# Optimization experiments

Hardware: AMD Instinct MI355X
Metric: run time of the kernel (lower is better)

Reference implementation:

```python
import jax, jax.numpy as jnp
import numpy as np

IOU_THR = 0.5
TOP_K = 10
D_MODEL = 256
BS, NQ = 8, 1000


def _layer_norm(x, g, b, eps=1e-5):
    m = x.mean(-1, keepdims=True)
    v = ((x - m) ** 2).mean(-1, keepdims=True)
    return (x - m) * jax.lax.rsqrt(v + eps) * g + b


def _box_iou(boxes):
    # boxes: [nq, 4] xyxy; pairwise IoU [nq, nq]
    area = (boxes[:, 2] - boxes[:, 0]) * (boxes[:, 3] - boxes[:, 1])
    lt = jnp.maximum(boxes[:, None, :2], boxes[None, :, :2])
    rb = jnp.minimum(boxes[:, None, 2:], boxes[None, :, 2:])
    wh = jnp.clip(rb - lt, 0.0)
    inter = wh[..., 0] * wh[..., 1]
    union = area[:, None] + area[None, :] - inter
    return inter / union


def setup_inputs() -> dict:
    key = jax.random.key(0)
    ks = jax.random.split(key, 16)
    d = D_MODEL
    s = 1.0 / np.sqrt(d)
    tgt = jax.random.normal(ks[0], (BS, NQ, d), dtype=jnp.float32)
    seed_mask = (jax.random.uniform(ks[1], (BS, NQ, 1)) < 0.2).astype(jnp.float32)
    # cxcywh boxes in (0,1) with positive wh
    cxy = jax.random.uniform(ks[2], (BS, NQ, 2), minval=0.1, maxval=0.9)
    wh = jax.random.uniform(ks[3], (BS, NQ, 2), minval=0.05, maxval=0.3)
    pred_boxes = jnp.concatenate([cxy, wh], axis=-1).astype(jnp.float32)
    def lin(k):
        kw, kb = jax.random.split(k)
        return (jax.random.uniform(kw, (d, d), minval=-s, maxval=s, dtype=jnp.float32),
                jax.random.uniform(kb, (d,), minval=-s, maxval=s, dtype=jnp.float32))
    W1, b1 = lin(ks[4]); W2, b2 = lin(ks[5]); W3, b3 = lin(ks[6])
    W4, b4 = lin(ks[7]); W5, b5 = lin(ks[8])
    g2 = jnp.ones((d,), jnp.float32); be2 = jnp.zeros((d,), jnp.float32)
    return {"tgt": tgt, "seed_mask": seed_mask, "pred_boxes": pred_boxes,
            "W1": W1, "b1": b1, "W2": W2, "b2": b2, "g2": g2, "be2": be2,
            "W3": W3, "b3": b3, "W4": W4, "b4": b4, "W5": W5, "b5": b5}


def reference(tgt, seed_mask, pred_boxes, W1, b1, W2, b2, g2, be2, W3, b3, W4, b4, W5, b5):
    bs, nq, d = tgt.shape
    # cxcywh -> xyxy
    cxy, wh = pred_boxes[..., :2], pred_boxes[..., 2:]
    box_xyxy = jnp.concatenate([cxy - 0.5 * wh, cxy + 0.5 * wh], axis=-1)
    ious = jax.vmap(_box_iou)(box_xyxy)                       # [bs,nq,nq]
    attn_mask = ious >= IOU_THR
    neg_mask = 1.0 - seed_mask                                # [bs,nq,1]
    # mask out non-seed columns and seed rows
    overlaps = ious * jnp.swapaxes(seed_mask, 1, 2) * neg_mask  # [bs,nq,nq]
    idx = jnp.argsort(-overlaps, axis=-1)[..., :TOP_K]        # [bs,nq,k]
    nmk = jnp.take_along_axis(
        jnp.broadcast_to(jnp.swapaxes(seed_mask, 1, 2), (bs, nq, nq)), idx, axis=2)
    ious_g = jnp.take_along_axis(overlaps, idx, axis=2)       # [bs,nq,k]
    mk = nmk * (ious_g >= IOU_THR).astype(tgt.dtype)          # [bs,nq,k]
    # id token MLP + layernorm
    id_token = _layer_norm(jax.nn.relu(tgt @ W1 + b1) @ W2 + b2, g2, be2)
    # neighbor gather: [bs,nq,k,d]
    neighbors_id = jax.vmap(lambda t, i: t[i])(id_token, idx)
    id_feature = id_token[:, :, None, :] - neighbors_id
    features = jax.nn.relu(id_feature @ W3 + b3) @ W4 + b4
    cur_tgt = (features * mk[..., None]).max(axis=2)          # [bs,nq,d]
    cur_tgt = tgt + jax.nn.relu(cur_tgt @ W5 + b5) * neg_mask
    return cur_tgt, attn_mask
```

## Files before the change

### kernel.cpp

```cpp
#include <hip/hip_runtime.h>
#include <hip/hip_bf16.h>

#define BSZ   8
#define NQ    1000
#define DM    256
#define MROWS (BSZ*NQ)
#define TOPK  10

typedef __attribute__((ext_vector_type(8))) short short8;
typedef __attribute__((ext_vector_type(4))) float f32x4;
typedef unsigned short u16;
typedef unsigned int   u32;

static __device__ __forceinline__ float b2f(u16 u) { return __uint_as_float(((u32)u) << 16); }
static __device__ __forceinline__ u16 f2b(float f) {
    __hip_bfloat16 h = __float2bfloat16(f);
    return *(u16*)&h;
}
static __device__ __forceinline__ u32 encf(float f) {
    u32 u = __float_as_uint(f);
    return (u & 0x80000000u) ? ~u : (u | 0x80000000u);
}
static __device__ __forceinline__ float decf(u32 e) {
    u32 u = (e & 0x80000000u) ? (e ^ 0x80000000u) : ~e;
    return __uint_as_float(u);
}

__global__ __launch_bounds__(256) void prep_iou_k(
    const float* __restrict__ boxes, const float* __restrict__ seed,
    const float* __restrict__ W1, const float* __restrict__ W2,
    const float* __restrict__ W3, const float* __restrict__ W4,
    const float* __restrict__ W5, u16* __restrict__ WT,
    float* __restrict__ attn, int* __restrict__ cnt,
    int* __restrict__ inc0, int* __restrict__ idxs)
{
#pragma clang fp contract(off)
    if (blockIdx.x < 80) {
        const int m  = blockIdx.x >> 4;
        const int kb = (blockIdx.x & 15) * 16;
        const float* W = (m==0)?W1:(m==1)?W2:(m==2)?W3:(m==3)?W4:W5;
        u16* D = WT + (size_t)m * DM * DM;
        const int t = threadIdx.x;
        u16 tmp[16];
        #pragma unroll
        for (int kk = 0; kk < 16; ++kk)
            tmp[kk] = f2b(W[(size_t)(kb+kk)*DM + t]);
        #pragma unroll
        for (int kk = 0; kk < 16; ++kk)
            D[(size_t)t*DM + kb + kk] = tmp[kk];
        return;
    }

    __shared__ float sv[NQ];
    __shared__ int   sj[NQ];
    __shared__ int   scount;
    const int t   = threadIdx.x;
    const int row = blockIdx.x - 80;
    const int b   = row / NQ;
    if (t == 0) scount = 0;

    const float* bi = boxes + (size_t)row * 4;
    const float icx = bi[0], icy = bi[1], iw = bi[2], ih = bi[3];
    const float ix0 = icx - 0.5f*iw, iy0 = icy - 0.5f*ih;
    const float ix1 = icx + 0.5f*iw, iy1 = icy + 0.5f*ih;
    const float area_i = (ix1-ix0)*(iy1-iy0);
    const float neg_i  = 1.f - seed[row];
    __syncthreads();

    float* arow = attn + (size_t)row * NQ;
    for (int j = t; j < NQ; j += 256) {
        const float* bj = boxes + (size_t)(b*NQ + j) * 4;
        const float cx = bj[0], cy = bj[1], w = bj[2], h = bj[3];
        const float x0 = cx - 0.5f*w, y0 = cy - 0.5f*h;
        const float x1 = cx + 0.5f*w, y1 = cy + 0.5f*h;
        const float area_j = (x1-x0)*(y1-y0);
        const float ltx = fmaxf(ix0, x0), lty = fmaxf(iy0, y0);
        const float rbx = fminf(ix1, x1), rby = fminf(iy1, y1);
        const float wx = fmaxf(rbx-ltx, 0.f), wy = fmaxf(rby-lty, 0.f);
        const float inter = wx*wy;
        const float uni = (area_i + area_j) - inter;
        const float iou = inter / uni;
        arow[j] = (iou >= 0.5f) ? 1.0f : 0.0f;
        const float ov = (iou * seed[b*NQ + j]) * neg_i;
        if (ov >= 0.5f) {
            const int p = atomicAdd(&scount, 1);
            if (p < NQ) { sv[p] = ov; sj[p] = j; }
        }
    }
    __syncthreads();

    if (t == 0) {
        const int n = scount;
        inc0[row] = (n < TOPK) ? 1 : 0;
        if (n <= TOPK) {
            cnt[row] = n;
            for (int k = 0; k < n; ++k) idxs[row*TOPK + k] = b*NQ + sj[k];
        } else {
            float bv[TOPK]; int bj[TOPK];
            #pragma unroll
            for (int k = 0; k < TOPK; ++k) { bv[k] = -1.f; bj[k] = 0x7fffffff; }
            for (int e = 0; e < n; ++e) {
                const float v = sv[e]; const int j = sj[e];
                int w = 0;
                #pragma unroll
                for (int k = 1; k < TOPK; ++k)
                    if (bv[k] < bv[w] || (bv[k] == bv[w] && bj[k] > bj[w])) w = k;
                if (v > bv[w] || (v == bv[w] && j < bj[w])) { bv[w] = v; bj[w] = j; }
            }
            cnt[row] = TOPK;
            for (int k = 0; k < TOPK; ++k) idxs[row*TOPK + k] = b*NQ + bj[k];
        }
    }
}

template<int EPI>
static __device__ __forceinline__ void block_gemm256(
    const u16 (*__restrict__ A)[264], const u16* __restrict__ WT,
    const float* __restrict__ bias, u16 (*__restrict__ OutL)[264],
    u16* __restrict__ OutG, float* __restrict__ OutF,
    const float* __restrict__ tgt, const float* __restrict__ seed,
    int r0, u16 (*__restrict__ W_lds)[72], int t)
{
    const int lane = t & 63, wave = t >> 6;
    const int m = lane & 15, quad = lane >> 4;
    f32x4 acc[4];
    #pragma unroll
    for (int nt = 0; nt < 4; ++nt)
        #pragma unroll
        for (int i = 0; i < 4; ++i) acc[nt][i] = 0.f;
    for (int kc = 0; kc < 4; ++kc) {
        __syncthreads();
        #pragma unroll
        for (int pass = 0; pass < 8; ++pass) {
            const int n = pass*32 + (t >> 3), ko = (t & 7) * 8;
            *(uint4*)&W_lds[n][ko] = *(const uint4*)&WT[(size_t)n*DM + kc*64 + ko];
        }
        __syncthreads();
        #pragma unroll
        for (int ks = 0; ks < 2; ++ks) {
            const short8 a = *(const short8*)&A[m][kc*64 + ks*32 + quad*8];
            #pragma unroll
            for (int nt = 0; nt < 4; ++nt) {
                const int n = wave*64 + nt*16 + m;
                const short8 b = *(const short8*)&W_lds[n][ks*32 + quad*8];
                acc[nt] = __builtin_amdgcn_mfma_f32_16x16x32_bf16(a, b, acc[nt], 0, 0, 0);
            }
        }
    }
    #pragma unroll
    for (int nt = 0; nt < 4; ++nt) {
        const int n = wave*64 + nt*16 + m;
        const float bb = bias ? bias[n] : 0.f;
        #pragma unroll
        for (int reg = 0; reg < 4; ++reg) {
            const int rl = quad*4 + reg;
            float v = acc[nt][reg] + bb;
            if (EPI == 0) OutL[rl][n] = f2b(fmaxf(v, 0.f));
            if (EPI == 1) OutL[rl][n] = f2b(v);
            if (EPI == 2) OutG[(size_t)(r0+rl)*DM + n] = f2b(v);
            if (EPI == 3) {
                const int R = r0 + rl;
                OutF[(size_t)R*DM + n] = tgt[(size_t)R*DM + n]
                                       + fmaxf(v, 0.f) * (1.f - seed[R]);
            }
        }
    }
}

__global__ __launch_bounds__(256) void mlp_k(
    const float* __restrict__ tgt, const u16* __restrict__ WT,
    const float* __restrict__ b1, const float* __restrict__ b2,
    const float* __restrict__ g2, const float* __restrict__ be2,
    u16* __restrict__ P)
{
    __shared__ __align__(16) u16 bufA[16][264];
    __shared__ __align__(16) u16 bufB[16][264];
    __shared__ __align__(16) u16 W_lds[256][72];
    const int t = threadIdx.x, r0 = blockIdx.x * 16;
    const int lane = t & 63, wave = t >> 6;

    {
        const int r = t >> 4, c0 = (t & 15) * 16;
        const float* src = &tgt[(size_t)(r0 + r)*DM + c0];
        u16 h[16];
        #pragma unroll
        for (int q = 0; q < 4; ++q) {
            const float4 f = *(const float4*)&src[q*4];
            h[q*4+0] = f2b(f.x); h[q*4+1] = f2b(f.y);
            h[q*4+2] = f2b(f.z); h[q*4+3] = f2b(f.w);
        }
        *(uint4*)&bufA[r][c0]     = *(uint4*)&h[0];
        *(uint4*)&bufA[r][c0 + 8] = *(uint4*)&h[8];
    }
    const u16* W1T = WT;
    const u16* W2T = WT + (size_t)1*DM*DM;
    const u16* W3T = WT + (size_t)2*DM*DM;

    block_gemm256<0>(bufA, W1T, b1, bufB, nullptr, nullptr, nullptr, nullptr, r0, W_lds, t);
    block_gemm256<1>(bufB, W2T, b2, bufA, nullptr, nullptr, nullptr, nullptr, r0, W_lds, t);
    __syncthreads();
    for (int rr = 0; rr < 4; ++rr) {
        const int row = wave*4 + rr;
        float x[4];
        #pragma unroll
        for (int i = 0; i < 4; ++i) x[i] = b2f(bufA[row][lane + 64*i]);
        float s = x[0]+x[1]+x[2]+x[3];
        float q = x[0]*x[0]+x[1]*x[1]+x[2]*x[2]+x[3]*x[3];
        #pragma unroll
        for (int off = 32; off; off >>= 1) {
            s += __shfl_down(s, off, 64);
            q += __shfl_down(q, off, 64);
        }
        s = __shfl(s, 0, 64); q = __shfl(q, 0, 64);
        const float mn  = s * (1.f/DM);
        const float vr  = q * (1.f/DM) - mn*mn;
        const float inv = rsqrtf(vr + 1e-5f);
        #pragma unroll
        for (int i = 0; i < 4; ++i) {
            const int c = lane + 64*i;
            bufA[row][c] = f2b((x[i]-mn)*inv*g2[c] + be2[c]);
        }
    }
    block_gemm256<2>(bufA, W3T, nullptr, nullptr, P, nullptr, nullptr, nullptr, r0, W_lds, t);
}

__global__ __launch_bounds__(256) void pairs_final_k(
    const u16* __restrict__ P, const u16* __restrict__ WT,
    const float* __restrict__ b3, const float* __restrict__ b4,
    const float* __restrict__ b5,
    const int* __restrict__ cnt, const int* __restrict__ inc0,
    const int* __restrict__ idxs,
    const float* __restrict__ tgt, const float* __restrict__ seed,
    float* __restrict__ out)
{
    __shared__ __align__(16) u16 U[16][264];
    __shared__ __align__(16) u16 W_lds[256][72];
    __shared__ u32 cmU[16][264];
    __shared__ int pl_rl[176], pl_j[176];
    __shared__ int sInc[16];
    __shared__ int np;
    const int t = threadIdx.x, r0 = blockIdx.x * 16;
    const int lane = t & 63, wave = t >> 6;
    const int m = lane & 15, quad = lane >> 4;
    const u16* W4T = WT + (size_t)3*DM*DM;
    const u16* W5T = WT + (size_t)4*DM*DM;

    if (t == 0) np = 0;
    __syncthreads();
    if (t < 16) {
        const int r = r0 + t;
        int c = cnt[r];
        c = (c < 0) ? 0 : ((c > TOPK) ? TOPK : c);
        sInc[t] = inc0[r];
        const int base = atomicAdd(&np, c);
        for (int k = 0; k < c; ++k) {
            pl_rl[base + k] = t;
            int j = idxs[r*TOPK + k];
            j = (j < 0) ? 0 : ((j >= MROWS) ? MROWS-1 : j);
            pl_j[base + k] = j;
        }
    }
    __syncthreads();
    const int npairs = np;
    #pragma unroll
    for (int rl2 = 0; rl2 < 16; ++rl2)
        cmU[rl2][t] = sInc[rl2] ? 0x80000000u  : encf(-3.402823466e38f);
    const float bb3 = b3[t];

    for (int pc = 0; pc*16 < npairs; ++pc) {
        #pragma unroll
        for (int pp = 0; pp < 16; ++pp) {
            const int pr = pc*16 + pp;
            u16 uv = 0;
            if (pr < npairs) {
                const int i = r0 + pl_rl[pr];
                const int j = pl_j[pr];
                uv = f2b(fmaxf(b2f(P[(size_t)i*DM + t]) - b2f(P[(size_t)j*DM + t]) + bb3, 0.f));
            }
            U[pp][t] = uv;
        }
        f32x4 acc[4];
        #pragma unroll
        for (int nt = 0; nt < 4; ++nt)
            #pragma unroll
            for (int i = 0; i < 4; ++i) acc[nt][i] = 0.f;
        for (int kc = 0; kc < 4; ++kc) {
            __syncthreads();
            #pragma unroll
            for (int pass = 0; pass < 8; ++pass) {
                const int n = pass*32 + (t >> 3), ko = (t & 7) * 8;
                *(uint4*)&W_lds[n][ko] = *(const uint4*)&W4T[(size_t)n*DM + kc*64 + ko];
            }
            __syncthreads();
            #pragma unroll
            for (int ks = 0; ks < 2; ++ks) {
                const short8 a = *(const short8*)&U[m][kc*64 + ks*32 + quad*8];
                #pragma unroll
                for (int nt = 0; nt < 4; ++nt) {
                    const int n = wave*64 + nt*16 + m;
                    const short8 b = *(const short8*)&W_lds[n][ks*32 + quad*8];
                    acc[nt] = __builtin_amdgcn_mfma_f32_16x16x32_bf16(a, b, acc[nt], 0, 0, 0);
                }
            }
        }
        #pragma unroll
        for (int nt = 0; nt < 4; ++nt) {
            const int n = wave*64 + nt*16 + m;
            const float bb4 = b4[n];
            #pragma unroll
            for (int reg = 0; reg < 4; ++reg) {
                const int pr = pc*16 + quad*4 + reg;
                if (pr < npairs) {
                    const int rl2 = pl_rl[pr];
                    atomicMax(&cmU[rl2][n], encf(acc[nt][reg] + bb4));
                }
            }
        }
    }
    __syncthreads();
    #pragma unroll
    for (int rl2 = 0; rl2 < 16; ++rl2)
        U[rl2][t] = f2b(decf(cmU[rl2][t]));
    block_gemm256<3>(U, W5T, b5, nullptr, nullptr, out, tgt, seed, r0, W_lds, t);
}

extern "C" void kernel_launch(void* const* d_in, const int* in_sizes, int n_in,
                              void* d_out, int out_size, void* d_ws, size_t ws_size,
                              hipStream_t stream)
{
    (void)in_sizes; (void)n_in; (void)out_size; (void)ws_size;
    const float* tgt   = (const float*)d_in[0];
    const float* seed  = (const float*)d_in[1];
    const float* boxes = (const float*)d_in[2];
    const float* W1 = (const float*)d_in[3];
    const float* b1 = (const float*)d_in[4];
    const float* W2 = (const float*)d_in[5];
    const float* b2 = (const float*)d_in[6];
    const float* g2 = (const float*)d_in[7];
    const float* be2= (const float*)d_in[8];
    const float* W3 = (const float*)d_in[9];
    const float* b3 = (const float*)d_in[10];
    const float* W4 = (const float*)d_in[11];
    const float* b4 = (const float*)d_in[12];
    const float* W5 = (const float*)d_in[13];
    const float* b5 = (const float*)d_in[14];

    float* out_tgt  = (float*)d_out;
    float* out_attn = out_tgt + (size_t)MROWS * DM;

    u16* WT   = (u16*)d_ws;
    u16* P    = WT + (size_t)5*DM*DM;
    int* cnt  = (int*)(P + (size_t)MROWS*DM);
    int* inc0 = cnt + MROWS;
    int* idxs = inc0 + MROWS;

    prep_iou_k<<<80 + MROWS, 256, 0, stream>>>(boxes, seed, W1, W2, W3, W4, W5,
                                               WT, out_attn, cnt, inc0, idxs);
    mlp_k<<<MROWS/16, 256, 0, stream>>>(tgt, WT, b1, b2, g2, be2, P);
    pairs_final_k<<<MROWS/16, 256, 0, stream>>>(P, WT, b3, b4, b5, cnt, inc0, idxs,
                                                tgt, seed, out_tgt);
}
```

Measured before the change: 141.7 us.

## Run IoU/top-k blocks concurrently with MLP blocks in one fused launch

Moves the weight transpose into its own small kernel and merges the per-row IoU/top-k work with the id-token MLP into one launch whose blocks branch on block index, sharing a union-style shared-memory buffer. The aim is to overlap the latency-bound IoU blocks with the MFMA-heavy MLP tiles instead of running them in series. The trade-off is that shared-memory footprint per block becomes the MLP size for the IoU blocks too, which may reduce occupancy for the 8000 IoU blocks.

```diff
diff --git a/kernel.cpp b/kernel.cpp
--- a/kernel.cpp
+++ b/kernel.cpp
@@ -6,6 +6,7 @@
 #define DM    256
 #define MROWS (BSZ*NQ)
 #define TOPK  10
+#define NTILE (MROWS/16)
 
 typedef __attribute__((ext_vector_type(8))) short short8;
 typedef __attribute__((ext_vector_type(4))) float f32x4;
@@ -26,91 +27,23 @@
     return __uint_as_float(u);
 }
 
-__global__ __launch_bounds__(256) void prep_iou_k(
-    const float* __restrict__ boxes, const float* __restrict__ seed,
+__global__ __launch_bounds__(256) void prep_k(
     const float* __restrict__ W1, const float* __restrict__ W2,
     const float* __restrict__ W3, const float* __restrict__ W4,
-    const float* __restrict__ W5, u16* __restrict__ WT,
-    float* __restrict__ attn, int* __restrict__ cnt,
-    int* __restrict__ inc0, int* __restrict__ idxs)
-{
-#pragma clang fp contract(off)
-    if (blockIdx.x < 80) {
-        const int m  = blockIdx.x >> 4;
-        const int kb = (blockIdx.x & 15) * 16;
-        const float* W = (m==0)?W1:(m==1)?W2:(m==2)?W3:(m==3)?W4:W5;
-        u16* D = WT + (size_t)m * DM * DM;
-        const int t = threadIdx.x;
-        u16 tmp[16];
-        #pragma unroll
-        for (int kk = 0; kk < 16; ++kk)
-            tmp[kk] = f2b(W[(size_t)(kb+kk)*DM + t]);
-        #pragma unroll
-        for (int kk = 0; kk < 16; ++kk)
-            D[(size_t)t*DM + kb + kk] = tmp[kk];
-        return;
-    }
-
-    __shared__ float sv[NQ];
-    __shared__ int   sj[NQ];
-    __shared__ int   scount;
-    const int t   = threadIdx.x;
-    const int row = blockIdx.x - 80;
-    const int b   = row / NQ;
-    if (t == 0) scount = 0;
-
-    const float* bi = boxes + (size_t)row * 4;
-    const float icx = bi[0], icy = bi[1], iw = bi[2], ih = bi[3];
-    const float ix0 = icx - 0.5f*iw, iy0 = icy - 0.5f*ih;
-    const float ix1 = icx + 0.5f*iw, iy1 = icy + 0.5f*ih;
-    const float area_i = (ix1-ix0)*(iy1-iy0);
-    const float neg_i  = 1.f - seed[row];
-    __syncthreads();
-
-    float* arow = attn + (size_t)row * NQ;
-    for (int j = t; j < NQ; j += 256) {
-        const float* bj = boxes + (size_t)(b*NQ + j) * 4;
-        const float cx = bj[0], cy = bj[1], w = bj[2], h = bj[3];
-        const float x0 = cx - 0.5f*w, y0 = cy - 0.5f*h;
-        const float x1 = cx + 0.5f*w, y1 = cy + 0.5f*h;
-        const float area_j = (x1-x0)*(y1-y0);
-        const float ltx = fmaxf(ix0, x0), lty = fmaxf(iy0, y0);
-        const float rbx = fminf(ix1, x1), rby = fminf(iy1, y1);
-        const float wx = fmaxf(rbx-ltx, 0.f), wy = fmaxf(rby-lty, 0.f);
-        const float inter = wx*wy;
-        const float uni = (area_i + area_j) - inter;
-        const float iou = inter / uni;
-        arow[j] = (iou >= 0.5f) ? 1.0f : 0.0f;
-        const float ov = (iou * seed[b*NQ + j]) * neg_i;
-        if (ov >= 0.5f) {
-            const int p = atomicAdd(&scount, 1);
-            if (p < NQ) { sv[p] = ov; sj[p] = j; }
-        }
-    }
-    __syncthreads();
-
-    if (t == 0) {
-        const int n = scount;
-        inc0[row] = (n < TOPK) ? 1 : 0;
-        if (n <= TOPK) {
-            cnt[row] = n;
-            for (int k = 0; k < n; ++k) idxs[row*TOPK + k] = b*NQ + sj[k];
-        } else {
-            float bv[TOPK]; int bj[TOPK];
-            #pragma unroll
-            for (int k = 0; k < TOPK; ++k) { bv[k] = -1.f; bj[k] = 0x7fffffff; }
-            for (int e = 0; e < n; ++e) {
-                const float v = sv[e]; const int j = sj[e];
-                int w = 0;
-                #pragma unroll
-                for (int k = 1; k < TOPK; ++k)
-                    if (bv[k] < bv[w] || (bv[k] == bv[w] && bj[k] > bj[w])) w = k;
-                if (v > bv[w] || (v == bv[w] && j < bj[w])) { bv[w] = v; bj[w] = j; }
-            }
-            cnt[row] = TOPK;
-            for (int k = 0; k < TOPK; ++k) idxs[row*TOPK + k] = b*NQ + bj[k];
-        }
-    }
+    const float* __restrict__ W5, u16* __restrict__ WT)
+{
+    const int m  = blockIdx.x >> 4;
+    const int kb = (blockIdx.x & 15) * 16;
+    const float* W = (m==0)?W1:(m==1)?W2:(m==2)?W3:(m==3)?W4:W5;
+    u16* D = WT + (size_t)m * DM * DM;
+    const int t = threadIdx.x;
+    u16 tmp[16];
+    #pragma unroll
+    for (int kk = 0; kk < 16; ++kk)
+        tmp[kk] = f2b(W[(size_t)(kb+kk)*DM + t]);
+    #pragma unroll
+    for (int kk = 0; kk < 16; ++kk)
+        D[(size_t)t*DM + kb + kk] = tmp[kk];
 }
 
 template<int EPI>
@@ -167,61 +100,136 @@
     }
 }
 
-__global__ __launch_bounds__(256) void mlp_k(
-    const float* __restrict__ tgt, const u16* __restrict__ WT,
+struct MlpSmem { u16 bufA[16][264]; u16 bufB[16][264]; u16 W_lds[256][72]; };
+struct IouSmem { float sv[NQ]; int sj[NQ]; int scount; };
+
+__global__ __launch_bounds__(256) void fused_iou_mlp_k(
+    const float* __restrict__ boxes, const float* __restrict__ seed,
+    const u16* __restrict__ WT,
     const float* __restrict__ b1, const float* __restrict__ b2,
     const float* __restrict__ g2, const float* __restrict__ be2,
-    u16* __restrict__ P)
-{
-    __shared__ __align__(16) u16 bufA[16][264];
-    __shared__ __align__(16) u16 bufB[16][264];
-    __shared__ __align__(16) u16 W_lds[256][72];
-    const int t = threadIdx.x, r0 = blockIdx.x * 16;
-    const int lane = t & 63, wave = t >> 6;
+    const float* __restrict__ tgt,
+    u16* __restrict__ P, float* __restrict__ attn,
+    int* __restrict__ cnt, int* __restrict__ inc0, int* __restrict__ idxs)
+{
+    __shared__ __align__(16) unsigned char smraw[sizeof(MlpSmem)];
+    const int t = threadIdx.x;
+    const int bid = blockIdx.x;
+
+    if (bid < NTILE) {
+        MlpSmem& sm = *reinterpret_cast<MlpSmem*>(smraw);
+        const int r0 = bid * 16;
+        const int lane = t & 63, wave = t >> 6;
+        const u16* W1T = WT;
+        const u16* W2T = WT + (size_t)1*DM*DM;
+        const u16* W3T = WT + (size_t)2*DM*DM;
+
+        {
+            const int r = t >> 4, c0 = (t & 15) * 16;
+            const float* src = &tgt[(size_t)(r0 + r)*DM + c0];
+            __align__(16) u16 h[16];
+            #pragma unroll
+            for (int q = 0; q < 4; ++q) {
+                const float4 f = *(const float4*)&src[q*4];
+                h[q*4+0] = f2b(f.x); h[q*4+1] = f2b(f.y);
+                h[q*4+2] = f2b(f.z); h[q*4+3] = f2b(f.w);
+            }
+            *(uint4*)&sm.bufA[r][c0]     = *(uint4*)&h[0];
+            *(uint4*)&sm.bufA[r][c0 + 8] = *(uint4*)&h[8];
+        }
+
+        block_gemm256<0>(sm.bufA, W1T, b1, sm.bufB,
+                         nullptr, nullptr, nullptr, nullptr, r0, sm.W_lds, t);
+        block_gemm256<1>(sm.bufB, W2T, b2, sm.bufA,
+                         nullptr, nullptr, nullptr, nullptr, r0, sm.W_lds, t);
+        __syncthreads();
+        for (int rr = 0; rr < 4; ++rr) {
+            const int row = wave*4 + rr;
+            float x[4];
+            #pragma unroll
+            for (int i = 0; i < 4; ++i) x[i] = b2f(sm.bufA[row][lane + 64*i]);
+            float s = x[0]+x[1]+x[2]+x[3];
+            float q = x[0]*x[0]+x[1]*x[1]+x[2]*x[2]+x[3]*x[3];
+            #pragma unroll
+            for (int off = 32; off; off >>= 1) {
+                s += __shfl_down(s, off, 64);
+                q += __shfl_down(q, off, 64);
+            }
+            s = __shfl(s, 0, 64); q = __shfl(q, 0, 64);
+            const float mn  = s * (1.f/DM);
+            const float vr  = q * (1.f/DM) - mn*mn;
+            const float inv = rsqrtf(vr + 1e-5f);
+            #pragma unroll
+            for (int i = 0; i < 4; ++i) {
+                const int c = lane + 64*i;
+                sm.bufA[row][c] = f2b((x[i]-mn)*inv*g2[c] + be2[c]);
+            }
+        }
+        block_gemm256<2>(sm.bufA, W3T, nullptr, nullptr,
+                         P, nullptr, nullptr, nullptr, r0, sm.W_lds, t);
+        return;
+    }
 
     {
-        const int r = t >> 4, c0 = (t & 15) * 16;
-        const float* src = &tgt[(size_t)(r0 + r)*DM + c0];
-        u16 h[16];
-        #pragma unroll
-        for (int q = 0; q < 4; ++q) {
-            const float4 f = *(const float4*)&src[q*4];
-            h[q*4+0] = f2b(f.x); h[q*4+1] = f2b(f.y);
-            h[q*4+2] = f2b(f.z); h[q*4+3] = f2b(f.w);
-        }
-        *(uint4*)&bufA[r][c0]     = *(uint4*)&h[0];
-        *(uint4*)&bufA[r][c0 + 8] = *(uint4*)&h[8];
-    }
-    const u16* W1T = WT;
-    const u16* W2T = WT + (size_t)1*DM*DM;
-    const u16* W3T = WT + (size_t)2*DM*DM;
-
-    block_gemm256<0>(bufA, W1T, b1, bufB, nullptr, nullptr, nullptr, nullptr, r0, W_lds, t);
-    block_gemm256<1>(bufB, W2T, b2, bufA, nullptr, nullptr, nullptr, nullptr, r0, W_lds, t);
-    __syncthreads();
-    for (int rr = 0; rr < 4; ++rr) {
-        const int row = wave*4 + rr;
-        float x[4];
-        #pragma unroll
-        for (int i = 0; i < 4; ++i) x[i] = b2f(bufA[row][lane + 64*i]);
-        float s = x[0]+x[1]+x[2]+x[3];
-        float q = x[0]*x[0]+x[1]*x[1]+x[2]*x[2]+x[3]*x[3];
-        #pragma unroll
-        for (int off = 32; off; off >>= 1) {
-            s += __shfl_down(s, off, 64);
-            q += __shfl_down(q, off, 64);
-        }
-        s = __shfl(s, 0, 64); q = __shfl(q, 0, 64);
-        const float mn  = s * (1.f/DM);
-        const float vr  = q * (1.f/DM) - mn*mn;
-        const float inv = rsqrtf(vr + 1e-5f);
-        #pragma unroll
-        for (int i = 0; i < 4; ++i) {
-            const int c = lane + 64*i;
-            bufA[row][c] = f2b((x[i]-mn)*inv*g2[c] + be2[c]);
-        }
-    }
-    block_gemm256<2>(bufA, W3T, nullptr, nullptr, P, nullptr, nullptr, nullptr, r0, W_lds, t);
+        #pragma clang fp contract(off)
+        IouSmem& sm = *reinterpret_cast<IouSmem*>(smraw);
+        const int row = bid - NTILE;
+        const int b   = row / NQ;
+        if (t == 0) sm.scount = 0;
+
+        const float* bi = boxes + (size_t)row * 4;
+        const float icx = bi[0], icy = bi[1], iw = bi[2], ih = bi[3];
+        const float ix0 = icx - 0.5f*iw, iy0 = icy - 0.5f*ih;
+        const float ix1 = icx + 0.5f*iw, iy1 = icy + 0.5f*ih;
+        const float area_i = (ix1-ix0)*(iy1-iy0);
+        const float neg_i  = 1.f - seed[row];
+        __syncthreads();
+
+        float* arow = attn + (size_t)row * NQ;
+        for (int j = t; j < NQ; j += 256) {
+            const float* bj = boxes + (size_t)(b*NQ + j) * 4;
+            const float cx = bj[0], cy = bj[1], w = bj[2], h = bj[3];
+            const float x0 = cx - 0.5f*w, y0 = cy - 0.5f*h;
+            const float x1 = cx + 0.5f*w, y1 = cy + 0.5f*h;
+            const float area_j = (x1-x0)*(y1-y0);
+            const float ltx = fmaxf(ix0, x0), lty = fmaxf(iy0, y0);
+            const float rbx = fminf(ix1, x1), rby = fminf(iy1, y1);
+            const float wx = fmaxf(rbx-ltx, 0.f), wy = fmaxf(rby-lty, 0.f);
+            const float inter = wx*wy;
+            const float uni = (area_i + area_j) - inter;
+            const float iou = inter / uni;
+            arow[j] = (iou >= 0.5f) ? 1.0f : 0.0f;
+            const float ov = (iou * seed[b*NQ + j]) * neg_i;
+            if (ov >= 0.5f) {
+                const int p = atomicAdd(&sm.scount, 1);
+                if (p < NQ) { sm.sv[p] = ov; sm.sj[p] = j; }
+            }
+        }
+        __syncthreads();
+
+        if (t == 0) {
+            const int n = sm.scount;
+            inc0[row] = (n < TOPK) ? 1 : 0;
+            if (n <= TOPK) {
+                cnt[row] = n;
+                for (int k = 0; k < n; ++k) idxs[row*TOPK + k] = b*NQ + sm.sj[k];
+            } else {
+                float bv[TOPK]; int bj[TOPK];
+                #pragma unroll
+                for (int k = 0; k < TOPK; ++k) { bv[k] = -1.f; bj[k] = 0x7fffffff; }
+                for (int e = 0; e < n; ++e) {
+                    const float v = sm.sv[e]; const int j = sm.sj[e];
+                    int w = 0;
+                    #pragma unroll
+                    for (int k = 1; k < TOPK; ++k)
+                        if (bv[k] < bv[w] || (bv[k] == bv[w] && bj[k] > bj[w])) w = k;
+                    if (v > bv[w] || (v == bv[w] && j < bj[w])) { bv[w] = v; bj[w] = j; }
+                }
+                cnt[row] = TOPK;
+                for (int k = 0; k < TOPK; ++k) idxs[row*TOPK + k] = b*NQ + bj[k];
+            }
+        }
+    }
 }
 
 __global__ __launch_bounds__(256) void pairs_final_k(
@@ -321,7 +329,8 @@
     #pragma unroll
     for (int rl2 = 0; rl2 < 16; ++rl2)
         U[rl2][t] = f2b(decf(cmU[rl2][t]));
-    block_gemm256<3>(U, W5T, b5, nullptr, nullptr, out, tgt, seed, r0, W_lds, t);
+    block_gemm256<3>(U, W5T, b5, nullptr, nullptr, out,
+                     tgt, seed, r0, W_lds, t);
 }
 
 extern "C" void kernel_launch(void* const* d_in, const int* in_sizes, int n_in,
@@ -354,9 +363,9 @@
     int* inc0 = cnt + MROWS;
     int* idxs = inc0 + MROWS;
 
-    prep_iou_k<<<80 + MROWS, 256, 0, stream>>>(boxes, seed, W1, W2, W3, W4, W5,
-                                               WT, out_attn, cnt, inc0, idxs);
-    mlp_k<<<MROWS/16, 256, 0, stream>>>(tgt, WT, b1, b2, g2, be2, P);
+    prep_k<<<80, 256, 0, stream>>>(W1, W2, W3, W4, W5, WT);
+    fused_iou_mlp_k<<<NTILE + MROWS, 256, 0, stream>>>(
+        boxes, seed, WT, b1, b2, g2, be2, tgt, P, out_attn, cnt, inc0, idxs);
     pairs_final_k<<<MROWS/16, 256, 0, stream>>>(P, WT, b3, b4, b5, cnt, inc0, idxs,
                                                 tgt, seed, out_tgt);
 }
```

Result: slower. 149.3 us (+5.4%).
